# Kernel optimization log

Measured on AMD Instinct MI355X. Metric: run time of the kernel, lower is better.

Reference implementation:

```python
import jax, jax.numpy as jnp
import numpy as np

NUM_FIELDS = 40
EMBED_DIM = 64
IN_SUB = 40
OUT_SUB = 40
BATCH = 256


def setup_inputs() -> dict:
    key = jax.random.key(0)
    k0, k1 = jax.random.split(key)
    B0 = jax.random.normal(k0, (BATCH, NUM_FIELDS, EMBED_DIM), dtype=jnp.float32)
    Bi = jax.random.normal(k1, (BATCH, IN_SUB, EMBED_DIM), dtype=jnp.float32)
    # parameters, initialized exactly as in the torch module
    W = jnp.tile(jnp.eye(EMBED_DIM, dtype=jnp.float32)[None], (OUT_SUB, 1, 1))  # (n, D, D)
    alpha = jnp.ones((NUM_FIELDS, IN_SUB, OUT_SUB), dtype=jnp.float32)          # (f, i, n)
    h = jnp.ones((OUT_SUB, EMBED_DIM, 1), dtype=jnp.float32)                    # (n, D, 1)
    return {"B0": B0, "Bi": Bi, "W": W, "alpha": alpha, "h": h}


def reference(B0, Bi, W, alpha, h):
    # Math of the original: fusion[b,n,D,d] = sum_{f,i} B0[b,f,D]*Bi[b,i,d]*alpha[f,i,n]
    # (equivalent to the 5D outer product contracted with alpha, but never
    #  materializes the (b,f,i,D,D) tensor).
    fusion = jnp.einsum('bfD,bid,fin->bnDd', B0, Bi, alpha)  # (b, n, D, D)
    # elementwise scale by W then project with h: out[b,n,D] = sum_d fusion*W*h
    out = jnp.einsum('bnDd,nDd,nd->bnD', fusion, W, h[..., 0])
    return out
```

## Files before the change

### kernel.cpp

```cpp
#include <hip/hip_runtime.h>
#include <hip/hip_bf16.h>

#define NF 40
#define NI 40
#define NN 40
#define ED 64
#define NB 256

typedef __attribute__((ext_vector_type(8))) short   short8;
typedef __attribute__((ext_vector_type(8))) __bf16  bf16x8;
typedef __attribute__((ext_vector_type(4))) float   f32x4;

__device__ __forceinline__ unsigned short f2bf(float x) {
    union { float f; unsigned u; } v; v.f = x;
    unsigned r = v.u + 0x7FFFu + ((v.u >> 16) & 1u);
    return (unsigned short)(r >> 16);
}

__device__ __forceinline__ bf16x8 ld_frag(const unsigned short* p) {
    return __builtin_bit_cast(bf16x8, *(const short8*)p);
}

__device__ __forceinline__ f32x4 mfma16(bf16x8 a, bf16x8 b, f32x4 c) {
    return __builtin_amdgcn_mfma_f32_16x16x32_bf16(a, b, c, 0, 0, 0);
}

#define WHP_N (64 * 64)
#define ALP_N (48 * 64)
#define BPB 2

__global__ __launch_bounds__(256) void gif_prep4(
        const float* __restrict__ W, const float* __restrict__ alpha,
        const float* __restrict__ h,
        unsigned short* __restrict__ whp, unsigned short* __restrict__ alp) {
    const int x = blockIdx.x;
    const int t = threadIdx.x;
    if (x < NN) {
        const int n = x;
        for (int idx = t; idx < 64 * 64; idx += 256) {
            int d = idx & 63;
            whp[n * WHP_N + idx] = f2bf(W[n * ED * ED + idx] * h[n * ED + d]);
        }
        for (int idx = t; idx < 8 * 64; idx += 256)
            alp[n * ALP_N + (40 + (idx >> 6)) * 64 + (idx & 63)] = 0;
        for (int idx = t; idx < 40 * 24; idx += 256) {
            int i = idx / 24, f = 40 + idx - i * 24;
            alp[n * ALP_N + i * 64 + f] = 0;
        }
    } else {
        const int f = x - NN;
        for (int idx = t; idx < NI * NN; idx += 256) {
            int i = idx / NN, n = idx - i * NN;
            alp[n * ALP_N + i * 64 + f] = f2bf(alpha[(f * NI + i) * NN + n]);
        }
    }
}

#define PSM 72
__global__ __launch_bounds__(256, 2) void gif_main8b(
        const float* __restrict__ B0, const float* __restrict__ Bi,
        const unsigned short* __restrict__ whp,
        const unsigned short* __restrict__ alp,
        float* __restrict__ out) {
    const int bg = blockIdx.x;
    const int ng = blockIdx.y;
    const int t = threadIdx.x;
    const int lane = t & 63, w = t >> 6;
    const int quad = lane >> 4, l15 = lane & 15, fo = quad * 8;
    const int n = ng * 4 + w;

    __shared__ __align__(16) unsigned short sBi[48 * PSM];
    __shared__ __align__(16) unsigned short sBT[64 * PSM];

    float4 rbi[3], rb0[3];
    {
        const float4* biv = (const float4*)(Bi + (size_t)(bg * BPB) * NI * ED);
        const float4* b0v = (const float4*)(B0 + (size_t)(bg * BPB) * NF * ED);
#pragma unroll
        for (int k = 0; k < 3; ++k) {
            const int c = t + k * 256;
            if (c < 640) { rbi[k] = biv[c]; rb0[k] = b0v[c]; }
        }
    }

    bf16x8 alA[3][2], whB[4][2];
    {
        const unsigned short* ap = alp + n * ALP_N;
        const unsigned short* wp = whp + n * WHP_N;
#pragma unroll
        for (int m = 0; m < 3; ++m)
#pragma unroll
            for (int s = 0; s < 2; ++s)
                alA[m][s] = ld_frag(&ap[(m * 16 + l15) * 64 + s * 32 + fo]);
#pragma unroll
        for (int tt = 0; tt < 4; ++tt)
#pragma unroll
            for (int s = 0; s < 2; ++s)
                whB[tt][s] = ld_frag(&wp[(tt * 16 + l15) * 64 + s * 32 + fo]);
    }

    for (int idx = t; idx < 8 * 64; idx += 256)
        sBi[(40 + (idx >> 6)) * PSM + (idx & 63)] = 0;
    for (int idx = t; idx < 64 * 24; idx += 256) {
        int D = idx / 24, f = 40 + idx - D * 24;
        sBT[D * PSM + f] = 0;
    }

#pragma unroll
    for (int k = 0; k < 3; ++k) {
        const int c = t + k * 256;
        if (c < 640) {
            const int r = c >> 4, col = (c & 15) * 4;
            ushort4 pk;
            pk.x = f2bf(rbi[k].x); pk.y = f2bf(rbi[k].y);
            pk.z = f2bf(rbi[k].z); pk.w = f2bf(rbi[k].w);
            *(ushort4*)&sBi[r * PSM + col] = pk;
            sBT[(col + 0) * PSM + r] = f2bf(rb0[k].x);
            sBT[(col + 1) * PSM + r] = f2bf(rb0[k].y);
            sBT[(col + 2) * PSM + r] = f2bf(rb0[k].z);
            sBT[(col + 3) * PSM + r] = f2bf(rb0[k].w);
        }
    }
    __syncthreads();

#pragma unroll
    for (int j = 0; j < BPB; ++j) {
        const int b = bg * BPB + j;

        if (j < BPB - 1) {
            const float4* biv = (const float4*)(Bi + (size_t)(b + 1) * NI * ED);
            const float4* b0v = (const float4*)(B0 + (size_t)(b + 1) * NF * ED);
#pragma unroll
            for (int k = 0; k < 3; ++k) {
                const int c = t + k * 256;
                if (c < 640) { rbi[k] = biv[c]; rb0[k] = b0v[c]; }
            }
        }

        bf16x8 biA[3][2];
#pragma unroll
        for (int m = 0; m < 3; ++m)
#pragma unroll
            for (int s = 0; s < 2; ++s)
                biA[m][s] = ld_frag(&sBi[(m * 16 + l15) * PSM + s * 32 + fo]);

        float p[4];
#pragma unroll
        for (int tt = 0; tt < 4; ++tt) {
            bf16x8 bb0 = ld_frag(&sBT[(tt * 16 + l15) * PSM + fo]);
            bf16x8 bb1 = ld_frag(&sBT[(tt * 16 + l15) * PSM + 32 + fo]);
            float acc = 0.f;
#pragma unroll
            for (int m = 0; m < 3; ++m) {
                f32x4 z = {0.f, 0.f, 0.f, 0.f};
                f32x4 T = mfma16(biA[m][0], whB[tt][0], z);
                T = mfma16(biA[m][1], whB[tt][1], T);
                f32x4 G = mfma16(alA[m][0], bb0, z);
                G = mfma16(alA[m][1], bb1, G);
                acc += T[0] * G[0] + T[1] * G[1] + T[2] * G[2] + T[3] * G[3];
            }
            p[tt] = acc;
        }
#pragma unroll
        for (int tt = 0; tt < 4; ++tt) {
            p[tt] += __shfl_xor(p[tt], 16, 64);
            p[tt] += __shfl_xor(p[tt], 32, 64);
        }
        float v = (quad == 0) ? p[0] : (quad == 1) ? p[1] : (quad == 2) ? p[2] : p[3];
        out[((size_t)b * NN + n) * ED + lane] = v;

        if (j < BPB - 1) {
            __syncthreads();
#pragma unroll
            for (int k = 0; k < 3; ++k) {
                const int c = t + k * 256;
                if (c < 640) {
                    const int r = c >> 4, col = (c & 15) * 4;
                    ushort4 pk;
                    pk.x = f2bf(rbi[k].x); pk.y = f2bf(rbi[k].y);
                    pk.z = f2bf(rbi[k].z); pk.w = f2bf(rbi[k].w);
                    *(ushort4*)&sBi[r * PSM + col] = pk;
                    sBT[(col + 0) * PSM + r] = f2bf(rb0[k].x);
                    sBT[(col + 1) * PSM + r] = f2bf(rb0[k].y);
                    sBT[(col + 2) * PSM + r] = f2bf(rb0[k].z);
                    sBT[(col + 3) * PSM + r] = f2bf(rb0[k].w);
                }
            }
            __syncthreads();
        }
    }
}

#define PS 72

__device__ __forceinline__ bf16x8 mk_al_frag(const float* __restrict__ alpha,
        int n, int m, int s, int l15, int quad) {
    bf16x8 r;
    const int row = m * 16 + l15;
    const int f0 = s * 32 + quad * 8;
#pragma unroll
    for (int j = 0; j < 8; ++j) {
        const int f = f0 + j;
        float v = (row < NI && f < NF) ? alpha[(f * NI + row) * NN + n] : 0.f;
        r[j] = (__bf16)v;
    }
    return r;
}
__device__ __forceinline__ bf16x8 mk_wh_frag(const float* __restrict__ W,
        const float* __restrict__ h, int n, int tt, int s, int l15, int quad) {
    bf16x8 r;
    const int row = tt * 16 + l15;
    const int k0 = s * 32 + quad * 8;
#pragma unroll
    for (int j = 0; j < 8; ++j) {
        float v = W[n * ED * ED + row * ED + k0 + j] * h[n * ED + k0 + j];
        r[j] = (__bf16)v;
    }
    return r;
}

__global__ __launch_bounds__(256) void gif_mfma(
        const float* __restrict__ B0, const float* __restrict__ Bi,
        const float* __restrict__ W, const float* __restrict__ alpha,
        const float* __restrict__ h, float* __restrict__ out) {
    const int q = blockIdx.x >> 8;
    const int b = blockIdx.x & 255;

    __shared__ __align__(16) unsigned short sBi[48 * PS];
    __shared__ __align__(16) unsigned short sBT[ED * PS];

    const int t = threadIdx.x;
    for (int idx = t; idx < 48 * PS; idx += 256) {
        int i = idx / PS, c = idx - i * PS;
        sBi[idx] = (i < NI && c < ED) ? f2bf(Bi[b * NI * ED + i * ED + c])
                                      : (unsigned short)0;
    }
    for (int idx = t; idx < ED * PS; idx += 256) {
        int D = idx / PS, c = idx - D * PS;
        sBT[idx] = (c < NF) ? f2bf(B0[b * NF * ED + c * ED + D])
                            : (unsigned short)0;
    }
    __syncthreads();

    const int lane = t & 63, w = t >> 6;
    const int quad = lane >> 4, l15 = lane & 15;
    const int fragoff = quad * 8;

    bf16x8 biA[3][2], b0B[4][2];
#pragma unroll
    for (int m = 0; m < 3; ++m)
#pragma unroll
        for (int s = 0; s < 2; ++s)
            biA[m][s] = ld_frag(&sBi[(m * 16 + l15) * PS + s * 32 + fragoff]);
#pragma unroll
    for (int tt = 0; tt < 4; ++tt)
#pragma unroll
        for (int s = 0; s < 2; ++s)
            b0B[tt][s] = ld_frag(&sBT[(tt * 16 + l15) * PS + s * 32 + fragoff]);

#pragma unroll
    for (int rep = 0; rep < 2; ++rep) {
        const int n = q * 8 + w + rep * 4;

        bf16x8 alA[3][2];
#pragma unroll
        for (int m = 0; m < 3; ++m)
#pragma unroll
            for (int s = 0; s < 2; ++s)
                alA[m][s] = mk_al_frag(alpha, n, m, s, l15, quad);

        float p[4];
#pragma unroll
        for (int tt = 0; tt < 4; ++tt) {
            bf16x8 whB2[2];
            whB2[0] = mk_wh_frag(W, h, n, tt, 0, l15, quad);
            whB2[1] = mk_wh_frag(W, h, n, tt, 1, l15, quad);
            float acc = 0.f;
#pragma unroll
            for (int m = 0; m < 3; ++m) {
                f32x4 z = {0.f, 0.f, 0.f, 0.f};
                f32x4 T = mfma16(biA[m][0], whB2[0], z);
                T = mfma16(biA[m][1], whB2[1], T);
                f32x4 G = mfma16(alA[m][0], b0B[tt][0], z);
                G = mfma16(alA[m][1], b0B[tt][1], G);
                acc += T[0] * G[0] + T[1] * G[1] + T[2] * G[2] + T[3] * G[3];
            }
            p[tt] = acc;
        }
#pragma unroll
        for (int tt = 0; tt < 4; ++tt) {
            p[tt] += __shfl_xor(p[tt], 16, 64);
            p[tt] += __shfl_xor(p[tt], 32, 64);
        }
        float v = (quad == 0) ? p[0] : (quad == 1) ? p[1] : (quad == 2) ? p[2] : p[3];
        out[(b * NN + n) * ED + lane] = v;
    }
}

extern "C" void kernel_launch(void* const* d_in, const int* in_sizes, int n_in,
                              void* d_out, int out_size, void* d_ws, size_t ws_size,
                              hipStream_t stream) {
    const float* B0    = (const float*)d_in[0];
    const float* Bi    = (const float*)d_in[1];
    const float* W     = (const float*)d_in[2];
    const float* alpha = (const float*)d_in[3];
    const float* h     = (const float*)d_in[4];
    float* out = (float*)d_out;

    const size_t need1 = (size_t)(NN * WHP_N + NN * ALP_N) * sizeof(unsigned short);
    if (ws_size >= need1) {
        unsigned short* whp = (unsigned short*)d_ws;
        unsigned short* alp = whp + (size_t)NN * WHP_N;
        gif_prep4<<<NN + NF, 256, 0, stream>>>(W, alpha, h, whp, alp);
        gif_main8b<<<dim3(NB / BPB, 10), 256, 0, stream>>>(B0, Bi, whp, alp, out);
        return;
    }

    gif_mfma<<<5 * NB, 256, 0, stream>>>(B0, Bi, W, alpha, h, out);
}
```

Baseline: 81.35 us.

## Fuse parameter prep into main kernel, dropping separate prep launch

Removes the separate prep kernel that packed W*h and a transposed alpha into bf16 workspace buffers. Each block of the main kernel now loads W and h directly into registers and multiplies and converts them to bf16 fragments. It also stages its 4-n slice of alpha, transposed and zero-padded, in shared memory. This removes one kernel launch and the workspace round trip. In exchange every block redoes the parameter conversion, and the larger shared footprint (about 24KB more) may lower occupancy.

```diff
diff --git a/kernel.cpp b/kernel.cpp
--- a/kernel.cpp
+++ b/kernel.cpp
@@ -25,43 +25,28 @@
     return __builtin_amdgcn_mfma_f32_16x16x32_bf16(a, b, c, 0, 0, 0);
 }
 
-#define WHP_N (64 * 64)
-#define ALP_N (48 * 64)
+__device__ __forceinline__ float4 mul4(const float4 a, const float4 b) {
+    float4 r; r.x = a.x * b.x; r.y = a.y * b.y; r.z = a.z * b.z; r.w = a.w * b.w;
+    return r;
+}
+
+__device__ __forceinline__ bf16x8 pack8(const float4 a, const float4 b) {
+    short8 s;
+    s[0] = (short)f2bf(a.x); s[1] = (short)f2bf(a.y);
+    s[2] = (short)f2bf(a.z); s[3] = (short)f2bf(a.w);
+    s[4] = (short)f2bf(b.x); s[5] = (short)f2bf(b.y);
+    s[6] = (short)f2bf(b.z); s[7] = (short)f2bf(b.w);
+    return __builtin_bit_cast(bf16x8, s);
+}
+
 #define BPB 2
-
-__global__ __launch_bounds__(256) void gif_prep4(
+#define PSM 72
+#define ALS (48 * 64)
+
+__global__ __launch_bounds__(256, 2) void gif_fused(
+        const float* __restrict__ B0, const float* __restrict__ Bi,
         const float* __restrict__ W, const float* __restrict__ alpha,
-        const float* __restrict__ h,
-        unsigned short* __restrict__ whp, unsigned short* __restrict__ alp) {
-    const int x = blockIdx.x;
-    const int t = threadIdx.x;
-    if (x < NN) {
-        const int n = x;
-        for (int idx = t; idx < 64 * 64; idx += 256) {
-            int d = idx & 63;
-            whp[n * WHP_N + idx] = f2bf(W[n * ED * ED + idx] * h[n * ED + d]);
-        }
-        for (int idx = t; idx < 8 * 64; idx += 256)
-            alp[n * ALP_N + (40 + (idx >> 6)) * 64 + (idx & 63)] = 0;
-        for (int idx = t; idx < 40 * 24; idx += 256) {
-            int i = idx / 24, f = 40 + idx - i * 24;
-            alp[n * ALP_N + i * 64 + f] = 0;
-        }
-    } else {
-        const int f = x - NN;
-        for (int idx = t; idx < NI * NN; idx += 256) {
-            int i = idx / NN, n = idx - i * NN;
-            alp[n * ALP_N + i * 64 + f] = f2bf(alpha[(f * NI + i) * NN + n]);
-        }
-    }
-}
-
-#define PSM 72
-__global__ __launch_bounds__(256, 2) void gif_main8b(
-        const float* __restrict__ B0, const float* __restrict__ Bi,
-        const unsigned short* __restrict__ whp,
-        const unsigned short* __restrict__ alp,
-        float* __restrict__ out) {
+        const float* __restrict__ h, float* __restrict__ out) {
     const int bg = blockIdx.x;
     const int ng = blockIdx.y;
     const int t = threadIdx.x;
@@ -71,6 +56,7 @@
 
     __shared__ __align__(16) unsigned short sBi[48 * PSM];
     __shared__ __align__(16) unsigned short sBT[64 * PSM];
+    __shared__ __align__(16) unsigned short sAl[4 * ALS];
 
     float4 rbi[3], rb0[3];
     {
@@ -83,20 +69,49 @@
         }
     }
 
-    bf16x8 alA[3][2], whB[4][2];
-    {
-        const unsigned short* ap = alp + n * ALP_N;
-        const unsigned short* wp = whp + n * WHP_N;
-#pragma unroll
-        for (int m = 0; m < 3; ++m)
-#pragma unroll
-            for (int s = 0; s < 2; ++s)
-                alA[m][s] = ld_frag(&ap[(m * 16 + l15) * 64 + s * 32 + fo]);
+    float4 wf[4][2][2];
+    float4 hv[2][2];
+    {
+        const float* wp = W + (size_t)n * ED * ED;
 #pragma unroll
         for (int tt = 0; tt < 4; ++tt)
 #pragma unroll
-            for (int s = 0; s < 2; ++s)
-                whB[tt][s] = ld_frag(&wp[(tt * 16 + l15) * 64 + s * 32 + fo]);
+            for (int s = 0; s < 2; ++s) {
+                const float* p = wp + (tt * 16 + l15) * ED + s * 32 + fo;
+                wf[tt][s][0] = *(const float4*)p;
+                wf[tt][s][1] = *(const float4*)(p + 4);
+            }
+#pragma unroll
+        for (int s = 0; s < 2; ++s) {
+            const float* p = h + n * ED + s * 32 + fo;
+            hv[s][0] = *(const float4*)p;
+            hv[s][1] = *(const float4*)(p + 4);
+        }
+    }
+
+    {
+        const float4* av = (const float4*)alpha;
+#pragma unroll
+        for (int k = 0; k < 7; ++k) {
+            const int e = t + k * 256;
+            if (e < NF * NI) {
+                const int f = e / NI, i = e - f * NI;
+                const float4 a4 = av[e * (NN / 4) + ng];
+                sAl[0 * ALS + i * 64 + f] = f2bf(a4.x);
+                sAl[1 * ALS + i * 64 + f] = f2bf(a4.y);
+                sAl[2 * ALS + i * 64 + f] = f2bf(a4.z);
+                sAl[3 * ALS + i * 64 + f] = f2bf(a4.w);
+            }
+        }
+        for (int idx = t; idx < 4 * 8 * 64; idx += 256) {
+            const int np = idx >> 9, rem = idx & 511;
+            sAl[np * ALS + (40 + (rem >> 6)) * 64 + (rem & 63)] = 0;
+        }
+        for (int idx = t; idx < 4 * 40 * 24; idx += 256) {
+            const int np = idx / 960, rem = idx - np * 960;
+            const int i = rem / 24, f = 40 + rem - i * 24;
+            sAl[np * ALS + i * 64 + f] = 0;
+        }
     }
 
     for (int idx = t; idx < 8 * 64; idx += 256)
@@ -105,7 +120,6 @@
         int D = idx / 24, f = 40 + idx - D * 24;
         sBT[D * PSM + f] = 0;
     }
-
 #pragma unroll
     for (int k = 0; k < 3; ++k) {
         const int c = t + k * 256;
@@ -122,6 +136,23 @@
         }
     }
     __syncthreads();
+
+    bf16x8 whB[4][2];
+#pragma unroll
+    for (int tt = 0; tt < 4; ++tt)
+#pragma unroll
+        for (int s = 0; s < 2; ++s)
+            whB[tt][s] = pack8(mul4(wf[tt][s][0], hv[s][0]),
+                               mul4(wf[tt][s][1], hv[s][1]));
+    bf16x8 alA[3][2];
+    {
+        const unsigned short* ap = &sAl[w * ALS];
+#pragma unroll
+        for (int m = 0; m < 3; ++m)
+#pragma unroll
+            for (int s = 0; s < 2; ++s)
+                alA[m][s] = ld_frag(&ap[(m * 16 + l15) * 64 + s * 32 + fo]);
+    }
 
 #pragma unroll
     for (int j = 0; j < BPB; ++j) {
@@ -191,112 +222,6 @@
     }
 }
 
-#define PS 72
-
-__device__ __forceinline__ bf16x8 mk_al_frag(const float* __restrict__ alpha,
-        int n, int m, int s, int l15, int quad) {
-    bf16x8 r;
-    const int row = m * 16 + l15;
-    const int f0 = s * 32 + quad * 8;
-#pragma unroll
-    for (int j = 0; j < 8; ++j) {
-        const int f = f0 + j;
-        float v = (row < NI && f < NF) ? alpha[(f * NI + row) * NN + n] : 0.f;
-        r[j] = (__bf16)v;
-    }
-    return r;
-}
-__device__ __forceinline__ bf16x8 mk_wh_frag(const float* __restrict__ W,
-        const float* __restrict__ h, int n, int tt, int s, int l15, int quad) {
-    bf16x8 r;
-    const int row = tt * 16 + l15;
-    const int k0 = s * 32 + quad * 8;
-#pragma unroll
-    for (int j = 0; j < 8; ++j) {
-        float v = W[n * ED * ED + row * ED + k0 + j] * h[n * ED + k0 + j];
-        r[j] = (__bf16)v;
-    }
-    return r;
-}
-
-__global__ __launch_bounds__(256) void gif_mfma(
-        const float* __restrict__ B0, const float* __restrict__ Bi,
-        const float* __restrict__ W, const float* __restrict__ alpha,
-        const float* __restrict__ h, float* __restrict__ out) {
-    const int q = blockIdx.x >> 8;
-    const int b = blockIdx.x & 255;
-
-    __shared__ __align__(16) unsigned short sBi[48 * PS];
-    __shared__ __align__(16) unsigned short sBT[ED * PS];
-
-    const int t = threadIdx.x;
-    for (int idx = t; idx < 48 * PS; idx += 256) {
-        int i = idx / PS, c = idx - i * PS;
-        sBi[idx] = (i < NI && c < ED) ? f2bf(Bi[b * NI * ED + i * ED + c])
-                                      : (unsigned short)0;
-    }
-    for (int idx = t; idx < ED * PS; idx += 256) {
-        int D = idx / PS, c = idx - D * PS;
-        sBT[idx] = (c < NF) ? f2bf(B0[b * NF * ED + c * ED + D])
-                            : (unsigned short)0;
-    }
-    __syncthreads();
-
-    const int lane = t & 63, w = t >> 6;
-    const int quad = lane >> 4, l15 = lane & 15;
-    const int fragoff = quad * 8;
-
-    bf16x8 biA[3][2], b0B[4][2];
-#pragma unroll
-    for (int m = 0; m < 3; ++m)
-#pragma unroll
-        for (int s = 0; s < 2; ++s)
-            biA[m][s] = ld_frag(&sBi[(m * 16 + l15) * PS + s * 32 + fragoff]);
-#pragma unroll
-    for (int tt = 0; tt < 4; ++tt)
-#pragma unroll
-        for (int s = 0; s < 2; ++s)
-            b0B[tt][s] = ld_frag(&sBT[(tt * 16 + l15) * PS + s * 32 + fragoff]);
-
-#pragma unroll
-    for (int rep = 0; rep < 2; ++rep) {
-        const int n = q * 8 + w + rep * 4;
-
-        bf16x8 alA[3][2];
-#pragma unroll
-        for (int m = 0; m < 3; ++m)
-#pragma unroll
-            for (int s = 0; s < 2; ++s)
-                alA[m][s] = mk_al_frag(alpha, n, m, s, l15, quad);
-
-        float p[4];
-#pragma unroll
-        for (int tt = 0; tt < 4; ++tt) {
-            bf16x8 whB2[2];
-            whB2[0] = mk_wh_frag(W, h, n, tt, 0, l15, quad);
-            whB2[1] = mk_wh_frag(W, h, n, tt, 1, l15, quad);
-            float acc = 0.f;
-#pragma unroll
-            for (int m = 0; m < 3; ++m) {
-                f32x4 z = {0.f, 0.f, 0.f, 0.f};
-                f32x4 T = mfma16(biA[m][0], whB2[0], z);
-                T = mfma16(biA[m][1], whB2[1], T);
-                f32x4 G = mfma16(alA[m][0], b0B[tt][0], z);
-                G = mfma16(alA[m][1], b0B[tt][1], G);
-                acc += T[0] * G[0] + T[1] * G[1] + T[2] * G[2] + T[3] * G[3];
-            }
-            p[tt] = acc;
-        }
-#pragma unroll
-        for (int tt = 0; tt < 4; ++tt) {
-            p[tt] += __shfl_xor(p[tt], 16, 64);
-            p[tt] += __shfl_xor(p[tt], 32, 64);
-        }
-        float v = (quad == 0) ? p[0] : (quad == 1) ? p[1] : (quad == 2) ? p[2] : p[3];
-        out[(b * NN + n) * ED + lane] = v;
-    }
-}
-
 extern "C" void kernel_launch(void* const* d_in, const int* in_sizes, int n_in,
                               void* d_out, int out_size, void* d_ws, size_t ws_size,
                               hipStream_t stream) {
@@ -307,14 +232,6 @@
     const float* h     = (const float*)d_in[4];
     float* out = (float*)d_out;
 
-    const size_t need1 = (size_t)(NN * WHP_N + NN * ALP_N) * sizeof(unsigned short);
-    if (ws_size >= need1) {
-        unsigned short* whp = (unsigned short*)d_ws;
-        unsigned short* alp = whp + (size_t)NN * WHP_N;
-        gif_prep4<<<NN + NF, 256, 0, stream>>>(W, alpha, h, whp, alp);
-        gif_main8b<<<dim3(NB / BPB, 10), 256, 0, stream>>>(B0, Bi, whp, alp, out);
-        return;
-    }
-
-    gif_mfma<<<5 * NB, 256, 0, stream>>>(B0, Bi, W, alpha, h, out);
-}
+    (void)d_ws; (void)ws_size;
+    gif_fused<<<dim3(NB / BPB, 10), 256, 0, stream>>>(B0, Bi, W, alpha, h, out);
+}
```

New measurement: 96.69 us. +18.9%, slower.

## Pre-convert B0/Bi to swizzled bf16 in prep kernel, copy straight to LDS

Applied to the files above, without the earlier changes.

The prep kernel gains one block per batch that converts B0 (transposed) and Bi to bf16 in an XOR-swizzled, zero-padded layout in workspace. The main kernel then loads both batches' tiles with 16-byte vector loads and copies them straight into LDS, removing the per-block fp32-to-bf16 conversion, the scattered transpose stores, and the mid-loop resync. This avoids redoing the conversion in each of the 10 n-group blocks that share a batch, at the cost of an extra global round trip for the bf16 copy. The swizzle is meant to avoid LDS bank conflicts without row padding.

```diff
diff --git a/kernel.cpp b/kernel.cpp
--- a/kernel.cpp
+++ b/kernel.cpp
@@ -27,12 +27,17 @@
 
 #define WHP_N (64 * 64)
 #define ALP_N (48 * 64)
+#define BFT_N 7168
+#define BI_OFF 0
+#define B0T_OFF (48 * 64)
 #define BPB 2
 
-__global__ __launch_bounds__(256) void gif_prep4(
+__global__ __launch_bounds__(256) void gif_prep5(
+        const float* __restrict__ B0, const float* __restrict__ Bi,
         const float* __restrict__ W, const float* __restrict__ alpha,
         const float* __restrict__ h,
-        unsigned short* __restrict__ whp, unsigned short* __restrict__ alp) {
+        unsigned short* __restrict__ whp, unsigned short* __restrict__ alp,
+        unsigned short* __restrict__ bft) {
     const int x = blockIdx.x;
     const int t = threadIdx.x;
     if (x < NN) {
@@ -47,20 +52,69 @@
             int i = idx / 24, f = 40 + idx - i * 24;
             alp[n * ALP_N + i * 64 + f] = 0;
         }
-    } else {
+    } else if (x < NN + NF) {
         const int f = x - NN;
         for (int idx = t; idx < NI * NN; idx += 256) {
             int i = idx / NN, n = idx - i * NN;
             alp[n * ALP_N + i * 64 + f] = f2bf(alpha[(f * NI + i) * NN + n]);
         }
-    }
-}
-
-#define PSM 72
-__global__ __launch_bounds__(256, 2) void gif_main8b(
-        const float* __restrict__ B0, const float* __restrict__ Bi,
+    } else {
+        const int b = x - (NN + NF);
+        unsigned short* dst = bft + (size_t)b * BFT_N;
+        __shared__ __align__(16) unsigned short sT[64 * 72];
+
+        const float4* biv = (const float4*)(Bi + (size_t)b * NI * ED);
+        const float4* b0v = (const float4*)(B0 + (size_t)b * NF * ED);
+        float4 rb[3], r0[3];
+#pragma unroll
+        for (int k = 0; k < 3; ++k) {
+            const int c = t + k * 256;
+            if (c < 640) { rb[k] = biv[c]; r0[k] = b0v[c]; }
+        }
+
+        for (int idx = t; idx < 64 * 32; idx += 256)
+            sT[(idx >> 5) * 72 + 40 + (idx & 31)] = 0;
+
+#pragma unroll
+        for (int k = 0; k < 3; ++k) {
+            const int c = t + k * 256;
+            if (c < 640) {
+                const int i = c >> 4, d0 = (c & 15) * 4;
+                ushort4 pk;
+                pk.x = f2bf(rb[k].x); pk.y = f2bf(rb[k].y);
+                pk.z = f2bf(rb[k].z); pk.w = f2bf(rb[k].w);
+                const int chunk = (d0 >> 3) ^ (i & 7);
+                *(ushort4*)&dst[BI_OFF + i * 64 + (chunk << 3) + (d0 & 7)] = pk;
+            }
+        }
+        for (int idx = t; idx < 8 * 64; idx += 256)
+            dst[BI_OFF + (40 + (idx >> 6)) * 64 + (idx & 63)] = 0;
+
+#pragma unroll
+        for (int k = 0; k < 3; ++k) {
+            const int c = t + k * 256;
+            if (c < 640) {
+                const int f = c >> 4, D0 = (c & 15) * 4;
+                sT[(D0 + 0) * 72 + f] = f2bf(r0[k].x);
+                sT[(D0 + 1) * 72 + f] = f2bf(r0[k].y);
+                sT[(D0 + 2) * 72 + f] = f2bf(r0[k].z);
+                sT[(D0 + 3) * 72 + f] = f2bf(r0[k].w);
+            }
+        }
+        __syncthreads();
+
+        for (int g = t; g < 512; g += 256) {
+            const int D = g >> 3, pc = g & 7;
+            short8 v = *(const short8*)&sT[D * 72 + ((pc ^ (D & 7)) << 3)];
+            *(short8*)&dst[B0T_OFF + D * 64 + (pc << 3)] = v;
+        }
+    }
+}
+
+__global__ __launch_bounds__(256, 2) void gif_main9(
         const unsigned short* __restrict__ whp,
         const unsigned short* __restrict__ alp,
+        const unsigned short* __restrict__ bft,
         float* __restrict__ out) {
     const int bg = blockIdx.x;
     const int ng = blockIdx.y;
@@ -69,19 +123,12 @@
     const int quad = lane >> 4, l15 = lane & 15, fo = quad * 8;
     const int n = ng * 4 + w;
 
-    __shared__ __align__(16) unsigned short sBi[48 * PSM];
-    __shared__ __align__(16) unsigned short sBT[64 * PSM];
-
-    float4 rbi[3], rb0[3];
-    {
-        const float4* biv = (const float4*)(Bi + (size_t)(bg * BPB) * NI * ED);
-        const float4* b0v = (const float4*)(B0 + (size_t)(bg * BPB) * NF * ED);
-#pragma unroll
-        for (int k = 0; k < 3; ++k) {
-            const int c = t + k * 256;
-            if (c < 640) { rbi[k] = biv[c]; rb0[k] = b0v[c]; }
-        }
-    }
+    __shared__ __align__(16) unsigned short sBuf[2 * BFT_N];
+
+    const short8* src = (const short8*)(bft + (size_t)(bg * BPB) * BFT_N);
+    short8 st[7];
+#pragma unroll
+    for (int k = 0; k < 7; ++k) st[k] = src[t + k * 256];
 
     bf16x8 alA[3][2], whB[4][2];
     {
@@ -99,56 +146,34 @@
                 whB[tt][s] = ld_frag(&wp[(tt * 16 + l15) * 64 + s * 32 + fo]);
     }
 
-    for (int idx = t; idx < 8 * 64; idx += 256)
-        sBi[(40 + (idx >> 6)) * PSM + (idx & 63)] = 0;
-    for (int idx = t; idx < 64 * 24; idx += 256) {
-        int D = idx / 24, f = 40 + idx - D * 24;
-        sBT[D * PSM + f] = 0;
-    }
-
-#pragma unroll
-    for (int k = 0; k < 3; ++k) {
-        const int c = t + k * 256;
-        if (c < 640) {
-            const int r = c >> 4, col = (c & 15) * 4;
-            ushort4 pk;
-            pk.x = f2bf(rbi[k].x); pk.y = f2bf(rbi[k].y);
-            pk.z = f2bf(rbi[k].z); pk.w = f2bf(rbi[k].w);
-            *(ushort4*)&sBi[r * PSM + col] = pk;
-            sBT[(col + 0) * PSM + r] = f2bf(rb0[k].x);
-            sBT[(col + 1) * PSM + r] = f2bf(rb0[k].y);
-            sBT[(col + 2) * PSM + r] = f2bf(rb0[k].z);
-            sBT[(col + 3) * PSM + r] = f2bf(rb0[k].w);
-        }
-    }
+#pragma unroll
+    for (int k = 0; k < 7; ++k)
+        *(short8*)&sBuf[(size_t)(t + k * 256) * 8] = st[k];
     __syncthreads();
 
 #pragma unroll
     for (int j = 0; j < BPB; ++j) {
+        const unsigned short* sb = &sBuf[j * BFT_N];
         const int b = bg * BPB + j;
 
-        if (j < BPB - 1) {
-            const float4* biv = (const float4*)(Bi + (size_t)(b + 1) * NI * ED);
-            const float4* b0v = (const float4*)(B0 + (size_t)(b + 1) * NF * ED);
-#pragma unroll
-            for (int k = 0; k < 3; ++k) {
-                const int c = t + k * 256;
-                if (c < 640) { rbi[k] = biv[c]; rb0[k] = b0v[c]; }
-            }
-        }
-
         bf16x8 biA[3][2];
 #pragma unroll
         for (int m = 0; m < 3; ++m)
 #pragma unroll
-            for (int s = 0; s < 2; ++s)
-                biA[m][s] = ld_frag(&sBi[(m * 16 + l15) * PSM + s * 32 + fo]);
+            for (int s = 0; s < 2; ++s) {
+                const int row = m * 16 + l15;
+                const int pch = ((s * 4 + quad) ^ (row & 7)) << 3;
+                biA[m][s] = ld_frag(&sb[BI_OFF + row * 64 + pch]);
+            }
 
         float p[4];
 #pragma unroll
         for (int tt = 0; tt < 4; ++tt) {
-            bf16x8 bb0 = ld_frag(&sBT[(tt * 16 + l15) * PSM + fo]);
-            bf16x8 bb1 = ld_frag(&sBT[(tt * 16 + l15) * PSM + 32 + fo]);
+            const int row = tt * 16 + l15;
+            const int pc0 = ((0 + quad) ^ (row & 7)) << 3;
+            const int pc1 = ((4 + quad) ^ (row & 7)) << 3;
+            bf16x8 bb0 = ld_frag(&sb[B0T_OFF + row * 64 + pc0]);
+            bf16x8 bb1 = ld_frag(&sb[B0T_OFF + row * 64 + pc1]);
             float acc = 0.f;
 #pragma unroll
             for (int m = 0; m < 3; ++m) {
@@ -168,26 +193,6 @@
         }
         float v = (quad == 0) ? p[0] : (quad == 1) ? p[1] : (quad == 2) ? p[2] : p[3];
         out[((size_t)b * NN + n) * ED + lane] = v;
-
-        if (j < BPB - 1) {
-            __syncthreads();
-#pragma unroll
-            for (int k = 0; k < 3; ++k) {
-                const int c = t + k * 256;
-                if (c < 640) {
-                    const int r = c >> 4, col = (c & 15) * 4;
-                    ushort4 pk;
-                    pk.x = f2bf(rbi[k].x); pk.y = f2bf(rbi[k].y);
-                    pk.z = f2bf(rbi[k].z); pk.w = f2bf(rbi[k].w);
-                    *(ushort4*)&sBi[r * PSM + col] = pk;
-                    sBT[(col + 0) * PSM + r] = f2bf(rb0[k].x);
-                    sBT[(col + 1) * PSM + r] = f2bf(rb0[k].y);
-                    sBT[(col + 2) * PSM + r] = f2bf(rb0[k].z);
-                    sBT[(col + 3) * PSM + r] = f2bf(rb0[k].w);
-                }
-            }
-            __syncthreads();
-        }
     }
 }
 
@@ -307,12 +312,15 @@
     const float* h     = (const float*)d_in[4];
     float* out = (float*)d_out;
 
-    const size_t need1 = (size_t)(NN * WHP_N + NN * ALP_N) * sizeof(unsigned short);
-    if (ws_size >= need1) {
+    const size_t need = (size_t)(NN * WHP_N + NN * ALP_N + NB * BFT_N)
+                        * sizeof(unsigned short);
+    if (ws_size >= need) {
         unsigned short* whp = (unsigned short*)d_ws;
         unsigned short* alp = whp + (size_t)NN * WHP_N;
-        gif_prep4<<<NN + NF, 256, 0, stream>>>(W, alpha, h, whp, alp);
-        gif_main8b<<<dim3(NB / BPB, 10), 256, 0, stream>>>(B0, Bi, whp, alp, out);
+        unsigned short* bft = alp + (size_t)NN * ALP_N;
+        gif_prep5<<<NN + NF + NB, 256, 0, stream>>>(B0, Bi, W, alpha, h,
+                                                    whp, alp, bft);
+        gif_main9<<<dim3(NB / BPB, 10), 256, 0, stream>>>(whp, alp, bft, out);
         return;
     }
 
```

New measurement: 79.86 us, median of 2. Within noise of the previous version (-1.8%).
